# Kernel tuning notes

Measured on AMD Instinct MI355X. Metric: run time of the kernel, lower is better.

The kernel has to match this reference:

```python
import jax, jax.numpy as jnp
import numpy as np

D_MODEL = 1024
K = 256
AMPLITUDE_MAX = 3.0
GATE_BIAS_INIT = 0.65  # alpha-gate bias initialized at logit(0.65)


def setup_inputs() -> dict:
    key = jax.random.key(0)
    k0, k1, k2, k3 = jax.random.split(key, 4)
    B, n = 4, 4096
    x = jax.random.normal(k0, (B, n, D_MODEL), dtype=jnp.float32)
    # OscillatorProjection: Linear(d_model -> 6K), chunks [A, omega, phi, alpha, g, beta]
    W_proj = jax.random.normal(k1, (6 * K, D_MODEL), dtype=jnp.float32) * 0.02
    b_proj = jnp.zeros((6 * K,), dtype=jnp.float32)
    alpha_bias = float(np.log(GATE_BIAS_INIT / (1.0 - GATE_BIAS_INIT)))
    b_proj = b_proj.at[3 * K:4 * K].set(alpha_bias)
    W_res = jax.random.normal(k2, (D_MODEL, 4 * K - 2), dtype=jnp.float32) * 0.002
    W_phase = jax.random.normal(k3, (K, D_MODEL), dtype=jnp.float32) * 0.001
    b_phase = jnp.zeros((K,), dtype=jnp.float32)
    return {
        "x": x, "W_proj": W_proj, "b_proj": b_proj, "W_res": W_res,
        "W_phase": W_phase, "b_phase": b_phase,
        "lambda_pcg": jnp.float32(0.1), "res_scale": jnp.float32(0.05),
    }


def _scan_combine(c1, c2):
    # first-order linear recurrence r_t = a_t * r_{t-1} + b_t (complex, split re/im)
    a1, br1, bi1 = c1
    a2, br2, bi2 = c2
    return (a1 * a2, a2 * br1 + br2, a2 * bi1 + bi2)


def _forward(x, W_proj, b_proj, W_res, W_phase, b_phase, lambda_pcg, res_scale):
    B, n, _ = x.shape
    # OscillatorProjection
    proj = jnp.einsum('bnd,kd->bnk', x, W_proj) + b_proj  # (B, n, 6K)
    a_raw, w_raw, p_raw, al_raw, g_raw, be_raw = jnp.split(proj, 6, axis=-1)
    A = AMPLITUDE_MAX * jax.nn.sigmoid(a_raw)
    omega = jax.nn.softplus(w_raw)
    phi = p_raw
    alpha = jax.nn.sigmoid(al_raw)
    g_out = jax.nn.sigmoid(g_raw)
    beta = jax.nn.sigmoid(be_raw)

    # phase_mode == 'log'
    positions = jnp.log1p(jnp.arange(n, dtype=jnp.float32)).reshape(1, n, 1)
    angle = omega * positions + phi
    cos_a = jnp.cos(angle)
    sin_a = jnp.sin(angle)
    one_m_a = 1.0 - alpha
    drive_r = one_m_a * A * cos_a
    drive_i = one_m_a * A * sin_a

    # parallel associative prefix scan over sequence axis
    _, r_r, r_i = jax.lax.associative_scan(_scan_combine, (alpha, drive_r, drive_i), axis=1)

    # erase (read-and-subtract)
    readout = r_r * cos_a + r_i * sin_a
    r_r = r_r - beta * readout * cos_a
    r_i = r_i - beta * readout * sin_a

    # state norm: r /= max(|r|, 1)
    modulus = jnp.sqrt(r_r * r_r + r_i * r_i + 1e-8)
    scale = jnp.maximum(modulus, 1.0)
    r_r = r_r / scale
    r_i = r_i / scale

    # demodulate: rho = r * exp(-j * angle)
    rho_re = r_r * cos_a + r_i * sin_a
    rho_im = -r_r * sin_a + r_i * cos_a

    # phase-coherence gate
    rho_norm = jnp.sqrt(rho_re * rho_re + rho_im * rho_im + 1e-8)
    phase_query = jnp.einsum('bnd,kd->bnk', x, W_phase) + b_phase
    phase_alignment = (rho_re / rho_norm) * jnp.cos(phase_query) + (rho_im / rho_norm) * jnp.sin(phase_query)
    phase_gate = jax.nn.sigmoid(lambda_pcg * phase_alignment)
    rho_re = phase_gate * rho_re
    rho_im = phase_gate * rho_im

    # SCPM: neighbor complex cross-products
    xcross_re = rho_re[:, :, :-1] * rho_re[:, :, 1:] - rho_im[:, :, :-1] * rho_im[:, :, 1:]
    xcross_im = rho_re[:, :, :-1] * rho_im[:, :, 1:] + rho_im[:, :, :-1] * rho_re[:, :, 1:]
    rho_base = jnp.concatenate([rho_re, rho_im], axis=-1)              # (B, n, 2K)
    g_base = jnp.concatenate([g_out, g_out], axis=-1)
    g_cross = 0.5 * (g_out[:, :, :-1] + g_out[:, :, 1:])
    xcross = jnp.concatenate([xcross_re, xcross_im], axis=-1)          # (B, n, 2K-2)
    g_cross_full = jnp.concatenate([g_cross, g_cross], axis=-1)
    rho = jnp.concatenate([g_base * rho_base, g_cross_full * xcross], axis=-1)  # (B, n, 4K-2)

    # eval mode: warmup_factor == 1.0
    return res_scale * jnp.einsum('bnk,dk->bnd', rho, W_res)


def reference(x, W_proj, b_proj, W_res, W_phase, b_phase, lambda_pcg, res_scale):
    return _forward(x, W_proj, b_proj, W_res, W_phase, b_phase, lambda_pcg, res_scale)
```

## Files before the change

### kernel.cpp

```cpp
#include <hip/hip_runtime.h>
#include <cmath>

#define D_MODEL 1024
#define KOSC    256
#define NSEQ    4096
#define BATCH   4
#define NROW    (BATCH * NSEQ)
#define JTOT    1792

typedef short      s16x8 __attribute__((ext_vector_type(8)));
typedef float      f32x4 __attribute__((ext_vector_type(4)));

#define GL2LDS(gsrc, ldst)                                                      \
  __builtin_amdgcn_global_load_lds(                                             \
      (const __attribute__((address_space(1))) unsigned int*)(gsrc),            \
      (__attribute__((address_space(3))) unsigned int*)(ldst), 16, 0, 0)

__device__ __forceinline__ float sigm(float x) {
    return 1.0f / (1.0f + expf(-x));
}
__device__ __forceinline__ float softplusf_(float x) {
    return fmaxf(x, 0.0f) + log1pf(expf(-fabsf(x)));
}

__device__ __forceinline__ void bf16_split(float f, unsigned short& hi,
                                           unsigned short& lo) {
    unsigned u = __float_as_uint(f);
    unsigned r = u + 0x7FFFu + ((u >> 16) & 1u);
    hi = (unsigned short)(r >> 16);
    float fh = __uint_as_float((unsigned)hi << 16);
    float fl = f - fh;
    unsigned ul = __float_as_uint(fl);
    unsigned rl = ul + 0x7FFFu + ((ul >> 16) & 1u);
    lo = (unsigned short)(rl >> 16);
}

__global__ __launch_bounds__(256) void split_x_kernel(
    const float* __restrict__ x, unsigned short* __restrict__ XH,
    unsigned short* __restrict__ XL)
{
    int i = blockIdx.x * 256 + threadIdx.x;
    float4 v = ((const float4*)x)[i];
    ushort4 h, l;
    bf16_split(v.x, h.x, l.x);
    bf16_split(v.y, h.y, l.y);
    bf16_split(v.z, h.z, l.z);
    bf16_split(v.w, h.w, l.w);
    ((ushort4*)XH)[i] = h;
    ((ushort4*)XL)[i] = l;
}

__global__ __launch_bounds__(256) void split_w_kernel(
    const float* __restrict__ Wproj, const float* __restrict__ Wphase,
    unsigned short* __restrict__ WH, unsigned short* __restrict__ WL)
{
    int i = blockIdx.x * 256 + threadIdx.x;
    int elem = i << 2;
    int row = elem >> 10;
    int col = elem & 1023;
    const float* src = (row < 1536) ? (Wproj + (size_t)row * 1024 + col)
                                    : (Wphase + (size_t)(row - 1536) * 1024 + col);
    float4 v = *(const float4*)src;
    ushort4 h, l;
    bf16_split(v.x, h.x, l.x);
    bf16_split(v.y, h.y, l.y);
    bf16_split(v.z, h.z, l.z);
    bf16_split(v.w, h.w, l.w);
    ((ushort4*)WH)[i] = h;
    ((ushort4*)WL)[i] = l;
}

__global__ __launch_bounds__(256) void pack_wres_kernel(
    const float* __restrict__ Wres, unsigned short* __restrict__ WPH)
{
    int idx = blockIdx.x * 256 + threadIdx.x;
    int d = idx >> 10;
    int j = idx & 1023;
    float v = (j < 1022) ? Wres[(size_t)d * 1022 + j] : 0.0f;
    unsigned u = __float_as_uint(v);
    unsigned r = u + 0x7FFFu + ((u >> 16) & 1u);
    WPH[idx] = (unsigned short)(r >> 16);
}

__global__ __launch_bounds__(256, 3) void gemm1_full_kernel(
    const unsigned short* __restrict__ WH, const unsigned short* __restrict__ WL,
    const unsigned short* __restrict__ XH, const unsigned short* __restrict__ XL,
    const float* __restrict__ bproj, float* __restrict__ PT)
{
    __shared__ __attribute__((aligned(16))) unsigned short AH[4096];
    __shared__ __attribute__((aligned(16))) unsigned short AL[4096];
    __shared__ __attribute__((aligned(16))) unsigned short BH[4096];
    __shared__ __attribute__((aligned(16))) unsigned short BL[4096];

    const int tid  = threadIdx.x;
    const int lane = tid & 63;
    const int w    = tid >> 6;
    const int wm   = w >> 1, wn = w & 1;
    const int m0   = (blockIdx.y + 2) * 128;
    const int n0   = blockIdx.x * 128;
    const int fr   = lane & 15;
    const int fq   = lane >> 4;

    f32x4 acc[4][4];
    #pragma unroll
    for (int i = 0; i < 4; i++)
        #pragma unroll
        for (int j = 0; j < 4; j++) acc[i][j] = (f32x4){0.f, 0.f, 0.f, 0.f};

    for (int kc = 0; kc < 32; kc++) {
        const int kbase = kc * 32;
        __syncthreads();
        #pragma unroll
        for (int t = 0; t < 2; t++) {
            int G  = w * 128 + t * 64 + lane;
            int gm = G & 127;
            int gq = G >> 7;
            size_t offA = (size_t)(m0 + gm) * 1024 + kbase + gq * 8;
            size_t offB = (size_t)(n0 + gm) * 1024 + kbase + gq * 8;
            int ldsg = (w * 128 + t * 64) * 8;
            GL2LDS(WH + offA, &AH[ldsg]);
            GL2LDS(WL + offA, &AL[ldsg]);
            GL2LDS(XH + offB, &BH[ldsg]);
            GL2LDS(XL + offB, &BL[ldsg]);
        }
        __syncthreads();

        s16x8 ah[4], al[4], bh[4], bl[4];
        #pragma unroll
        for (int f = 0; f < 4; f++) {
            int aoff = (fq * 128 + wm * 64 + f * 16 + fr) * 8;
            int boff = (fq * 128 + wn * 64 + f * 16 + fr) * 8;
            ah[f] = *(const s16x8*)&AH[aoff];
            al[f] = *(const s16x8*)&AL[aoff];
            bh[f] = *(const s16x8*)&BH[boff];
            bl[f] = *(const s16x8*)&BL[boff];
        }
        #pragma unroll
        for (int i = 0; i < 4; i++)
            #pragma unroll
            for (int j = 0; j < 4; j++) {
                acc[i][j] = __builtin_amdgcn_mfma_f32_16x16x32_bf16(ah[i], bh[j], acc[i][j], 0, 0, 0);
                acc[i][j] = __builtin_amdgcn_mfma_f32_16x16x32_bf16(ah[i], bl[j], acc[i][j], 0, 0, 0);
                acc[i][j] = __builtin_amdgcn_mfma_f32_16x16x32_bf16(al[i], bh[j], acc[i][j], 0, 0, 0);
            }
    }

    #pragma unroll
    for (int i = 0; i < 4; i++) {
        int mbase = m0 + wm * 64 + i * 16 + fq * 4;
        #pragma unroll
        for (int j = 0; j < 4; j++) {
            int n = n0 + wn * 64 + j * 16 + fr;
            #pragma unroll
            for (int rg = 0; rg < 4; rg++) {
                int m = mbase + rg;
                PT[(size_t)m * NROW + n] = acc[i][j][rg] + bproj[m];
            }
        }
    }
}

__global__ __launch_bounds__(256, 4) void gemm1_lite_kernel(
    const unsigned short* __restrict__ WH, const unsigned short* __restrict__ XH,
    const float* __restrict__ bproj, const float* __restrict__ bphase,
    float* __restrict__ PT)
{
    __shared__ __attribute__((aligned(16))) unsigned short AH[8192];
    __shared__ __attribute__((aligned(16))) unsigned short BH[8192];

    const int tid  = threadIdx.x;
    const int lane = tid & 63;
    const int w    = tid >> 6;
    const int wm   = w >> 1, wn = w & 1;
    const int yt   = blockIdx.y;
    const int jt   = (yt < 2) ? yt : yt + 4;
    const int m0   = jt * 128;
    const int n0   = blockIdx.x * 128;
    const int fr   = lane & 15;
    const int fq   = lane >> 4;

    f32x4 acc[4][4];
    #pragma unroll
    for (int i = 0; i < 4; i++)
        #pragma unroll
        for (int j = 0; j < 4; j++) acc[i][j] = (f32x4){0.f, 0.f, 0.f, 0.f};

    for (int kc = 0; kc < 16; kc++) {
        const int kbase = kc * 64;
        __syncthreads();
        #pragma unroll
        for (int t = 0; t < 4; t++) {
            int G  = t * 256 + tid;
            int gm = G & 127;
            int gq = G >> 7;
            size_t offA = (size_t)(m0 + gm) * 1024 + kbase + gq * 8;
            size_t offB = (size_t)(n0 + gm) * 1024 + kbase + gq * 8;
            int ldsg = (t * 256 + w * 64) * 8;
            GL2LDS(WH + offA, &AH[ldsg]);
            GL2LDS(XH + offB, &BH[ldsg]);
        }
        __syncthreads();

        #pragma unroll
        for (int s = 0; s < 2; s++) {
            s16x8 ah[4], bh[4];
            #pragma unroll
            for (int f = 0; f < 4; f++) {
                int aoff = (((s * 4 + fq) * 128) + wm * 64 + f * 16 + fr) * 8;
                int boff = (((s * 4 + fq) * 128) + wn * 64 + f * 16 + fr) * 8;
                ah[f] = *(const s16x8*)&AH[aoff];
                bh[f] = *(const s16x8*)&BH[boff];
            }
            #pragma unroll
            for (int i = 0; i < 4; i++)
                #pragma unroll
                for (int j = 0; j < 4; j++)
                    acc[i][j] = __builtin_amdgcn_mfma_f32_16x16x32_bf16(ah[i], bh[j], acc[i][j], 0, 0, 0);
        }
    }

    #pragma unroll
    for (int i = 0; i < 4; i++) {
        int mbase = m0 + wm * 64 + i * 16 + fq * 4;
        #pragma unroll
        for (int j = 0; j < 4; j++) {
            int n = n0 + wn * 64 + j * 16 + fr;
            #pragma unroll
            for (int rg = 0; rg < 4; rg++) {
                int m = mbase + rg;
                float bias = (m < 1536) ? bproj[m] : bphase[m - 1536];
                PT[(size_t)m * NROW + n] = acc[i][j][rg] + bias;
            }
        }
    }
}

__global__ __launch_bounds__(256) void scan_kernel(float* PT,
                                                   const float* lambda_ptr)
{
    const int bx = blockIdx.x;
    const int k = bx & 255;
    const int b = bx >> 8;
    const int t = threadIdx.x;
    const size_t colb = (size_t)b * NSEQ;
    const size_t R = NROW;

    float* rowA  = PT + (size_t)(k)        * R + colb;
    float* rowW  = PT + (size_t)(256 + k)  * R + colb;
    float* rowP  = PT + (size_t)(512 + k)  * R + colb;
    float* rowAl = PT + (size_t)(768 + k)  * R + colb;
    float* rowG  = PT + (size_t)(1024 + k) * R + colb;
    float* rowBe = PT + (size_t)(1280 + k) * R + colb;
    float* rowPq = PT + (size_t)(1536 + k) * R + colb;

    __shared__ float s_al[NSEQ + 256];
    __shared__ float s_rr[NSEQ + 256];
    __shared__ float s_ri[NSEQ + 256];
    __shared__ float s_sa[256], s_sbr[256], s_sbi[256];

    const float lam = *lambda_ptr;

    float cs_r[16], sn_r[16];

    #pragma unroll
    for (int i = 0; i < 16; i++) {
        int n = i * 256 + t;
        float araw = rowA[n];
        float wraw = rowW[n];
        float praw = rowP[n];
        float alraw = rowAl[n];
        float A     = 3.0f * sigm(araw);
        float alpha = sigm(alraw);
        float omega = softplusf_(wraw);
        float ang   = fmaf(omega, log1pf((float)n), praw);
        float sn, cs;
        sincosf(ang, &sn, &cs);
        cs_r[i] = cs;
        sn_r[i] = sn;
        float amp = (1.0f - alpha) * A;
        int pidx = n + (n >> 4);
        s_al[pidx] = alpha;
        s_rr[pidx] = amp * cs;
        s_ri[pidx] = amp * sn;
    }
    __syncthreads();

    {
        float ap = 1.0f, br = 0.0f, bi = 0.0f;
        int base = t * 17;
        #pragma unroll
        for (int i = 0; i < 16; i++) {
            float a = s_al[base + i];
            br = fmaf(a, br, s_rr[base + i]);
            bi = fmaf(a, bi, s_ri[base + i]);
            ap *= a;
        }
        s_sa[t] = ap; s_sbr[t] = br; s_sbi[t] = bi;
    }
    __syncthreads();

    for (int off = 1; off < 256; off <<= 1) {
        float a2 = s_sa[t], b2r = s_sbr[t], b2i = s_sbi[t];
        float a1 = 1.0f, b1r = 0.0f, b1i = 0.0f;
        if (t >= off) { a1 = s_sa[t - off]; b1r = s_sbr[t - off]; b1i = s_sbi[t - off]; }
        __syncthreads();
        s_sa[t]  = a1 * a2;
        s_sbr[t] = fmaf(a2, b1r, b2r);
        s_sbi[t] = fmaf(a2, b1i, b2i);
        __syncthreads();
    }

    {
        float cr = 0.0f, ci = 0.0f;
        if (t > 0) { cr = s_sbr[t - 1]; ci = s_sbi[t - 1]; }
        int base = t * 17;
        #pragma unroll
        for (int i = 0; i < 16; i++) {
            float a = s_al[base + i];
            cr = fmaf(a, cr, s_rr[base + i]);
            ci = fmaf(a, ci, s_ri[base + i]);
            s_rr[base + i] = cr;
            s_ri[base + i] = ci;
        }
    }
    __syncthreads();

    #pragma unroll
    for (int i = 0; i < 16; i++) {
        int n = i * 256 + t;
        float beraw = rowBe[n];
        float graw = rowG[n];
        float pq = rowPq[n];

        float cs = cs_r[i];
        float sn = sn_r[i];

        int pidx = n + (n >> 4);
        float rr = s_rr[pidx], ri = s_ri[pidx];
        float beta = sigm(beraw);
        float g = sigm(graw);

        float readout = rr * cs + ri * sn;
        rr -= beta * readout * cs;
        ri -= beta * readout * sn;

        float modulus = sqrtf(rr * rr + ri * ri + 1e-8f);
        float scale = fmaxf(modulus, 1.0f);
        rr /= scale; ri /= scale;

        float rho_re = rr * cs + ri * sn;
        float rho_im = -rr * sn + ri * cs;

        float rho_norm = sqrtf(rho_re * rho_re + rho_im * rho_im + 1e-8f);
        float sq, cq;
        sincosf(pq, &sq, &cq);
        float pa = (rho_re * cq + rho_im * sq) / rho_norm;
        float gate = sigm(lam * pa);
        rho_re *= gate;
        rho_im *= gate;

        rowA[n] = rho_re;
        rowW[n] = rho_im;
        rowP[n] = g;
    }
}

__global__ __launch_bounds__(256) void pack_rho_kernel(
    const float* __restrict__ PT, unsigned short* __restrict__ RTH,
    unsigned short* __restrict__ RTL)
{
    __shared__ float s_re[256 * 33];
    __shared__ float s_im[256 * 33];
    __shared__ float s_g [256 * 33];

    const int tid = threadIdx.x;
    const int r0 = blockIdx.x * 32;

    {
        int lr = tid & 31;
        int k0 = tid >> 5;
        for (int it = 0; it < 32; it++) {
            int k = it * 8 + k0;
            size_t go = (size_t)k * NROW + r0 + lr;
            s_re[k * 33 + lr] = PT[go];
            s_im[k * 33 + lr] = PT[(size_t)256 * NROW + go];
            s_g [k * 33 + lr] = PT[(size_t)512 * NROW + go];
        }
    }
    __syncthreads();

    const int r = tid >> 3;
    const int c = tid & 7;
    for (int i = 0; i < 16; i++) {
        int jb = (c + 8 * i) * 8;
        unsigned short h[8], l[8];
        #pragma unroll
        for (int e = 0; e < 8; e++) {
            int j = jb + e;
            float v;
            if (j < 256) {
                v = s_g[j * 33 + r] * s_re[j * 33 + r];
            } else if (j < 512) {
                int k = j - 256;
                v = s_g[k * 33 + r] * s_im[k * 33 + r];
            } else if (j < 767) {
                int k = j - 512;
                float gc = 0.5f * (s_g[k * 33 + r] + s_g[(k + 1) * 33 + r]);
                v = gc * (s_re[k * 33 + r] * s_re[(k + 1) * 33 + r]
                        - s_im[k * 33 + r] * s_im[(k + 1) * 33 + r]);
            } else if (j < 1022) {
                int k = j - 767;
                float gc = 0.5f * (s_g[k * 33 + r] + s_g[(k + 1) * 33 + r]);
                v = gc * (s_re[k * 33 + r] * s_im[(k + 1) * 33 + r]
                        + s_im[k * 33 + r] * s_re[(k + 1) * 33 + r]);
            } else {
                v = 0.0f;
            }
            bf16_split(v, h[e], l[e]);
        }
        size_t off = (size_t)(r0 + r) * 1024 + jb;
        s16x8 hv, lv;
        #pragma unroll
        for (int e = 0; e < 8; e++) { hv[e] = (short)h[e]; lv[e] = (short)l[e]; }
        *(s16x8*)&RTH[off] = hv;
        *(s16x8*)&RTL[off] = lv;
    }
}

__global__ __launch_bounds__(256, 3) void gemm2_kernel(
    const unsigned short* __restrict__ WPH,
    const unsigned short* __restrict__ RTH, const unsigned short* __restrict__ RTL,
    const float* __restrict__ rs_ptr, float* __restrict__ out)
{
    __shared__ __attribute__((aligned(16))) unsigned short AH[4096];
    __shared__ __attribute__((aligned(16))) unsigned short BH[4096];
    __shared__ __attribute__((aligned(16))) unsigned short BL[4096];

    const int tid  = threadIdx.x;
    const int lane = tid & 63;
    const int w    = tid >> 6;
    const int wm   = w >> 1, wn = w & 1;
    const int m0   = blockIdx.y * 128;
    const int n0   = blockIdx.x * 128;
    const int fr   = lane & 15;
    const int fq   = lane >> 4;
    const float rs = *rs_ptr;

    f32x4 acc[4][4];
    #pragma unroll
    for (int i = 0; i < 4; i++)
        #pragma unroll
        for (int j = 0; j < 4; j++) acc[i][j] = (f32x4){0.f, 0.f, 0.f, 0.f};

    for (int kc = 0; kc < 32; kc++) {
        const int kbase = kc * 32;
        __syncthreads();
        #pragma unroll
        for (int t = 0; t < 2; t++) {
            int G  = w * 128 + t * 64 + lane;
            int gm = G & 127;
            int gq = G >> 7;
            size_t offA = (size_t)(m0 + gm) * 1024 + kbase + gq * 8;
            size_t offB = (size_t)(n0 + gm) * 1024 + kbase + gq * 8;
            int ldsg = (w * 128 + t * 64) * 8;
            GL2LDS(WPH + offA, &AH[ldsg]);
            GL2LDS(RTH + offB, &BH[ldsg]);
            GL2LDS(RTL + offB, &BL[ldsg]);
        }
        __syncthreads();

        s16x8 ah[4], bh[4], bl[4];
        #pragma unroll
        for (int f = 0; f < 4; f++) {
            int aoff = (fq * 128 + wm * 64 + f * 16 + fr) * 8;
            int boff = (fq * 128 + wn * 64 + f * 16 + fr) * 8;
            ah[f] = *(const s16x8*)&AH[aoff];
            bh[f] = *(const s16x8*)&BH[boff];
            bl[f] = *(const s16x8*)&BL[boff];
        }
        #pragma unroll
        for (int i = 0; i < 4; i++)
            #pragma unroll
            for (int j = 0; j < 4; j++) {
                acc[i][j] = __builtin_amdgcn_mfma_f32_16x16x32_bf16(ah[i], bh[j], acc[i][j], 0, 0, 0);
                acc[i][j] = __builtin_amdgcn_mfma_f32_16x16x32_bf16(ah[i], bl[j], acc[i][j], 0, 0, 0);
            }
    }

    #pragma unroll
    for (int i = 0; i < 4; i++) {
        int d = m0 + wm * 64 + i * 16 + fq * 4;
        #pragma unroll
        for (int j = 0; j < 4; j++) {
            int n = n0 + wn * 64 + j * 16 + fr;
            float4 v = { rs * acc[i][j][0], rs * acc[i][j][1],
                         rs * acc[i][j][2], rs * acc[i][j][3] };
            *(float4*)&out[(size_t)n * 1024 + d] = v;
        }
    }
}

extern "C" void kernel_launch(void* const* d_in, const int* in_sizes, int n_in,
                              void* d_out, int out_size, void* d_ws, size_t ws_size,
                              hipStream_t stream)
{
    const float* x      = (const float*)d_in[0];
    const float* Wproj  = (const float*)d_in[1];
    const float* bproj  = (const float*)d_in[2];
    const float* Wres   = (const float*)d_in[3];
    const float* Wphase = (const float*)d_in[4];
    const float* bphase = (const float*)d_in[5];
    const float* lam    = (const float*)d_in[6];
    const float* rs     = (const float*)d_in[7];
    float* out = (float*)d_out;

    float* PT = (float*)d_ws;
    unsigned short* WH  = (unsigned short*)((char*)d_ws + (size_t)JTOT * NROW * 4);
    unsigned short* WL  = WH + (size_t)JTOT * 1024;
    unsigned short* RTH = (unsigned short*)(PT + (size_t)768 * NROW);
    unsigned short* RTL = RTH + (size_t)NROW * 1024;
    unsigned short* WPH = (unsigned short*)PT;
    unsigned short* XH  = (unsigned short*)d_out;
    unsigned short* XL  = XH + (size_t)NROW * 1024;

    hipLaunchKernelGGL(split_x_kernel, dim3(NROW * D_MODEL / 1024), dim3(256), 0, stream,
                       x, XH, XL);
    hipLaunchKernelGGL(split_w_kernel, dim3(JTOT * D_MODEL / 1024), dim3(256), 0, stream,
                       Wproj, Wphase, WH, WL);
    hipLaunchKernelGGL(gemm1_full_kernel, dim3(NROW / 128, 4), dim3(256), 0, stream,
                       WH, WL, XH, XL, bproj, PT);
    hipLaunchKernelGGL(gemm1_lite_kernel, dim3(NROW / 128, 10), dim3(256), 0, stream,
                       WH, XH, bproj, bphase, PT);
    hipLaunchKernelGGL(scan_kernel, dim3(BATCH * KOSC), dim3(256), 0, stream,
                       PT, lam);
    hipLaunchKernelGGL(pack_rho_kernel, dim3(NROW / 32), dim3(256), 0, stream,
                       PT, RTH, RTL);
    hipLaunchKernelGGL(pack_wres_kernel, dim3(1024 * 1024 / 256), dim3(256), 0, stream,
                       Wres, WPH);
    hipLaunchKernelGGL(gemm2_kernel, dim3(NROW / 128, 1024 / 128), dim3(256), 0, stream,
                       WPH, RTH, RTL, rs, out);
}
```

Before: 532.8 us.

## Double-buffer LDS tiles in all three GEMM kernels with MFMA priority boost

Switches the three MFMA GEMM kernels from single-buffered LDS staging, which had two barriers per k-step, to double buffering. The next k-tile is issued via global_load_lds while the current tile is consumed, leaving one barrier per step. s_setprio raises wave priority around the MFMA blocks. LDS use per block doubles and launch bounds drop to 2 blocks per CU, which lowers occupancy. Correctness relies on the async LDS loads completing before the end-of-iteration barrier.

```diff
diff --git a/kernel.cpp b/kernel.cpp
--- a/kernel.cpp
+++ b/kernel.cpp
@@ -82,15 +82,15 @@
     WPH[idx] = (unsigned short)(r >> 16);
 }
 
-__global__ __launch_bounds__(256, 3) void gemm1_full_kernel(
+__global__ __launch_bounds__(256, 2) void gemm1_full_kernel(
     const unsigned short* __restrict__ WH, const unsigned short* __restrict__ WL,
     const unsigned short* __restrict__ XH, const unsigned short* __restrict__ XL,
     const float* __restrict__ bproj, float* __restrict__ PT)
 {
-    __shared__ __attribute__((aligned(16))) unsigned short AH[4096];
-    __shared__ __attribute__((aligned(16))) unsigned short AL[4096];
-    __shared__ __attribute__((aligned(16))) unsigned short BH[4096];
-    __shared__ __attribute__((aligned(16))) unsigned short BL[4096];
+    __shared__ __attribute__((aligned(16))) unsigned short AH[8192];
+    __shared__ __attribute__((aligned(16))) unsigned short AL[8192];
+    __shared__ __attribute__((aligned(16))) unsigned short BH[8192];
+    __shared__ __attribute__((aligned(16))) unsigned short BL[8192];
 
     const int tid  = threadIdx.x;
     const int lane = tid & 63;
@@ -107,9 +107,8 @@
         #pragma unroll
         for (int j = 0; j < 4; j++) acc[i][j] = (f32x4){0.f, 0.f, 0.f, 0.f};
 
-    for (int kc = 0; kc < 32; kc++) {
+    auto STAGE = [&](int buf, int kc) {
         const int kbase = kc * 32;
-        __syncthreads();
         #pragma unroll
         for (int t = 0; t < 2; t++) {
             int G  = w * 128 + t * 64 + lane;
@@ -117,24 +116,32 @@
             int gq = G >> 7;
             size_t offA = (size_t)(m0 + gm) * 1024 + kbase + gq * 8;
             size_t offB = (size_t)(n0 + gm) * 1024 + kbase + gq * 8;
-            int ldsg = (w * 128 + t * 64) * 8;
+            int ldsg = buf * 4096 + (w * 128 + t * 64) * 8;
             GL2LDS(WH + offA, &AH[ldsg]);
             GL2LDS(WL + offA, &AL[ldsg]);
             GL2LDS(XH + offB, &BH[ldsg]);
             GL2LDS(XL + offB, &BL[ldsg]);
         }
-        __syncthreads();
+    };
+
+    STAGE(0, 0);
+    __syncthreads();
+
+    for (int kc = 0; kc < 32; kc++) {
+        const int cur = kc & 1;
+        if (kc + 1 < 32) STAGE(cur ^ 1, kc + 1);
 
         s16x8 ah[4], al[4], bh[4], bl[4];
         #pragma unroll
         for (int f = 0; f < 4; f++) {
-            int aoff = (fq * 128 + wm * 64 + f * 16 + fr) * 8;
-            int boff = (fq * 128 + wn * 64 + f * 16 + fr) * 8;
+            int aoff = cur * 4096 + (fq * 128 + wm * 64 + f * 16 + fr) * 8;
+            int boff = cur * 4096 + (fq * 128 + wn * 64 + f * 16 + fr) * 8;
             ah[f] = *(const s16x8*)&AH[aoff];
             al[f] = *(const s16x8*)&AL[aoff];
             bh[f] = *(const s16x8*)&BH[boff];
             bl[f] = *(const s16x8*)&BL[boff];
         }
+        __builtin_amdgcn_s_setprio(1);
         #pragma unroll
         for (int i = 0; i < 4; i++)
             #pragma unroll
@@ -143,6 +150,8 @@
                 acc[i][j] = __builtin_amdgcn_mfma_f32_16x16x32_bf16(ah[i], bl[j], acc[i][j], 0, 0, 0);
                 acc[i][j] = __builtin_amdgcn_mfma_f32_16x16x32_bf16(al[i], bh[j], acc[i][j], 0, 0, 0);
             }
+        __builtin_amdgcn_s_setprio(0);
+        __syncthreads();
     }
 
     #pragma unroll
@@ -160,13 +169,13 @@
     }
 }
 
-__global__ __launch_bounds__(256, 4) void gemm1_lite_kernel(
+__global__ __launch_bounds__(256, 2) void gemm1_lite_kernel(
     const unsigned short* __restrict__ WH, const unsigned short* __restrict__ XH,
     const float* __restrict__ bproj, const float* __restrict__ bphase,
     float* __restrict__ PT)
 {
-    __shared__ __attribute__((aligned(16))) unsigned short AH[8192];
-    __shared__ __attribute__((aligned(16))) unsigned short BH[8192];
+    __shared__ __attribute__((aligned(16))) unsigned short AH[16384];
+    __shared__ __attribute__((aligned(16))) unsigned short BH[16384];
 
     const int tid  = threadIdx.x;
     const int lane = tid & 63;
@@ -185,9 +194,8 @@
         #pragma unroll
         for (int j = 0; j < 4; j++) acc[i][j] = (f32x4){0.f, 0.f, 0.f, 0.f};
 
-    for (int kc = 0; kc < 16; kc++) {
+    auto STAGE = [&](int buf, int kc) {
         const int kbase = kc * 64;
-        __syncthreads();
         #pragma unroll
         for (int t = 0; t < 4; t++) {
             int G  = t * 256 + tid;
@@ -195,28 +203,38 @@
             int gq = G >> 7;
             size_t offA = (size_t)(m0 + gm) * 1024 + kbase + gq * 8;
             size_t offB = (size_t)(n0 + gm) * 1024 + kbase + gq * 8;
-            int ldsg = (t * 256 + w * 64) * 8;
+            int ldsg = buf * 8192 + (t * 256 + w * 64) * 8;
             GL2LDS(WH + offA, &AH[ldsg]);
             GL2LDS(XH + offB, &BH[ldsg]);
         }
-        __syncthreads();
+    };
+
+    STAGE(0, 0);
+    __syncthreads();
+
+    for (int kc = 0; kc < 16; kc++) {
+        const int cur = kc & 1;
+        if (kc + 1 < 16) STAGE(cur ^ 1, kc + 1);
 
         #pragma unroll
         for (int s = 0; s < 2; s++) {
             s16x8 ah[4], bh[4];
             #pragma unroll
             for (int f = 0; f < 4; f++) {
-                int aoff = (((s * 4 + fq) * 128) + wm * 64 + f * 16 + fr) * 8;
-                int boff = (((s * 4 + fq) * 128) + wn * 64 + f * 16 + fr) * 8;
+                int aoff = cur * 8192 + (((s * 4 + fq) * 128) + wm * 64 + f * 16 + fr) * 8;
+                int boff = cur * 8192 + (((s * 4 + fq) * 128) + wn * 64 + f * 16 + fr) * 8;
                 ah[f] = *(const s16x8*)&AH[aoff];
                 bh[f] = *(const s16x8*)&BH[boff];
             }
+            __builtin_amdgcn_s_setprio(1);
             #pragma unroll
             for (int i = 0; i < 4; i++)
                 #pragma unroll
                 for (int j = 0; j < 4; j++)
                     acc[i][j] = __builtin_amdgcn_mfma_f32_16x16x32_bf16(ah[i], bh[j], acc[i][j], 0, 0, 0);
-        }
+            __builtin_amdgcn_s_setprio(0);
+        }
+        __syncthreads();
     }
 
     #pragma unroll
@@ -432,9 +450,9 @@
     const unsigned short* __restrict__ RTH, const unsigned short* __restrict__ RTL,
     const float* __restrict__ rs_ptr, float* __restrict__ out)
 {
-    __shared__ __attribute__((aligned(16))) unsigned short AH[4096];
-    __shared__ __attribute__((aligned(16))) unsigned short BH[4096];
-    __shared__ __attribute__((aligned(16))) unsigned short BL[4096];
+    __shared__ __attribute__((aligned(16))) unsigned short AH[8192];
+    __shared__ __attribute__((aligned(16))) unsigned short BH[8192];
+    __shared__ __attribute__((aligned(16))) unsigned short BL[8192];
 
     const int tid  = threadIdx.x;
     const int lane = tid & 63;
@@ -452,9 +470,8 @@
         #pragma unroll
         for (int j = 0; j < 4; j++) acc[i][j] = (f32x4){0.f, 0.f, 0.f, 0.f};
 
-    for (int kc = 0; kc < 32; kc++) {
+    auto STAGE = [&](int buf, int kc) {
         const int kbase = kc * 32;
-        __syncthreads();
         #pragma unroll
         for (int t = 0; t < 2; t++) {
             int G  = w * 128 + t * 64 + lane;
@@ -462,22 +479,30 @@
             int gq = G >> 7;
             size_t offA = (size_t)(m0 + gm) * 1024 + kbase + gq * 8;
             size_t offB = (size_t)(n0 + gm) * 1024 + kbase + gq * 8;
-            int ldsg = (w * 128 + t * 64) * 8;
+            int ldsg = buf * 4096 + (w * 128 + t * 64) * 8;
             GL2LDS(WPH + offA, &AH[ldsg]);
             GL2LDS(RTH + offB, &BH[ldsg]);
             GL2LDS(RTL + offB, &BL[ldsg]);
         }
-        __syncthreads();
+    };
+
+    STAGE(0, 0);
+    __syncthreads();
+
+    for (int kc = 0; kc < 32; kc++) {
+        const int cur = kc & 1;
+        if (kc + 1 < 32) STAGE(cur ^ 1, kc + 1);
 
         s16x8 ah[4], bh[4], bl[4];
         #pragma unroll
         for (int f = 0; f < 4; f++) {
-            int aoff = (fq * 128 + wm * 64 + f * 16 + fr) * 8;
-            int boff = (fq * 128 + wn * 64 + f * 16 + fr) * 8;
+            int aoff = cur * 4096 + (fq * 128 + wm * 64 + f * 16 + fr) * 8;
+            int boff = cur * 4096 + (fq * 128 + wn * 64 + f * 16 + fr) * 8;
             ah[f] = *(const s16x8*)&AH[aoff];
             bh[f] = *(const s16x8*)&BH[boff];
             bl[f] = *(const s16x8*)&BL[boff];
         }
+        __builtin_amdgcn_s_setprio(1);
         #pragma unroll
         for (int i = 0; i < 4; i++)
             #pragma unroll
@@ -485,6 +510,8 @@
                 acc[i][j] = __builtin_amdgcn_mfma_f32_16x16x32_bf16(ah[i], bh[j], acc[i][j], 0, 0, 0);
                 acc[i][j] = __builtin_amdgcn_mfma_f32_16x16x32_bf16(ah[i], bl[j], acc[i][j], 0, 0, 0);
             }
+        __builtin_amdgcn_s_setprio(0);
+        __syncthreads();
     }
 
     #pragma unroll
```

New measurement: 534.2 us. About the same (+0.3%).

## Rewrite scan kernel with register-resident chunks and wavefront shuffle prefix scan

Applied to the files above, without the earlier changes.

Each thread now owns 16 contiguous sequence elements, loaded and stored as float4 vectors, and keeps them in registers instead of staging through LDS. The block-level Hillis-Steele scan with many __syncthreads is replaced by a 64-lane shuffle scan plus a small cross-wave combine through four shared slots. This removes most LDS traffic and barriers. It raises register pressure, which the launch bound of 3 blocks per unit tries to cap, at the risk of spills. Per-thread global accesses become strided by 16 elements rather than coalesced across threads.

```diff
diff --git a/kernel.cpp b/kernel.cpp
--- a/kernel.cpp
+++ b/kernel.cpp
@@ -235,110 +235,110 @@
     }
 }
 
-__global__ __launch_bounds__(256) void scan_kernel(float* PT,
-                                                   const float* lambda_ptr)
+__global__ __launch_bounds__(256, 3) void scan_kernel(float* PT,
+                                                      const float* lambda_ptr)
 {
     const int bx = blockIdx.x;
     const int k = bx & 255;
     const int b = bx >> 8;
     const int t = threadIdx.x;
+    const int lane = t & 63;
+    const int wv = t >> 6;
     const size_t colb = (size_t)b * NSEQ;
     const size_t R = NROW;
-
-    float* rowA  = PT + (size_t)(k)        * R + colb;
-    float* rowW  = PT + (size_t)(256 + k)  * R + colb;
-    float* rowP  = PT + (size_t)(512 + k)  * R + colb;
-    float* rowAl = PT + (size_t)(768 + k)  * R + colb;
-    float* rowG  = PT + (size_t)(1024 + k) * R + colb;
-    float* rowBe = PT + (size_t)(1280 + k) * R + colb;
-    float* rowPq = PT + (size_t)(1536 + k) * R + colb;
-
-    __shared__ float s_al[NSEQ + 256];
-    __shared__ float s_rr[NSEQ + 256];
-    __shared__ float s_ri[NSEQ + 256];
-    __shared__ float s_sa[256], s_sbr[256], s_sbi[256];
+    const int n0 = t * 16;
+
+    float* rowA  = PT + (size_t)(k)        * R + colb + n0;
+    float* rowW  = PT + (size_t)(256 + k)  * R + colb + n0;
+    float* rowP  = PT + (size_t)(512 + k)  * R + colb + n0;
+    float* rowAl = PT + (size_t)(768 + k)  * R + colb + n0;
+    float* rowG  = PT + (size_t)(1024 + k) * R + colb + n0;
+    float* rowBe = PT + (size_t)(1280 + k) * R + colb + n0;
+    float* rowPq = PT + (size_t)(1536 + k) * R + colb + n0;
+
+    __shared__ float s_a[4], s_br[4], s_bi[4];
 
     const float lam = *lambda_ptr;
 
-    float cs_r[16], sn_r[16];
-
+    float al_r[16], rr_r[16], ri_r[16], cs_r[16], sn_r[16];
+
+    float fa[16], fw[16], fp[16], fl[16];
+    #pragma unroll
+    for (int q = 0; q < 4; q++) {
+        *(float4*)&fa[q * 4] = ((const float4*)rowA)[q];
+        *(float4*)&fw[q * 4] = ((const float4*)rowW)[q];
+        *(float4*)&fp[q * 4] = ((const float4*)rowP)[q];
+        *(float4*)&fl[q * 4] = ((const float4*)rowAl)[q];
+    }
+    float ap = 1.0f, br = 0.0f, bi = 0.0f;
     #pragma unroll
     for (int i = 0; i < 16; i++) {
-        int n = i * 256 + t;
-        float araw = rowA[n];
-        float wraw = rowW[n];
-        float praw = rowP[n];
-        float alraw = rowAl[n];
-        float A     = 3.0f * sigm(araw);
-        float alpha = sigm(alraw);
-        float omega = softplusf_(wraw);
-        float ang   = fmaf(omega, log1pf((float)n), praw);
+        float A     = 3.0f * sigm(fa[i]);
+        float alpha = sigm(fl[i]);
+        float omega = softplusf_(fw[i]);
+        float ang   = fmaf(omega, log1pf((float)(n0 + i)), fp[i]);
         float sn, cs;
         sincosf(ang, &sn, &cs);
-        cs_r[i] = cs;
-        sn_r[i] = sn;
         float amp = (1.0f - alpha) * A;
-        int pidx = n + (n >> 4);
-        s_al[pidx] = alpha;
-        s_rr[pidx] = amp * cs;
-        s_ri[pidx] = amp * sn;
-    }
+        float dr = amp * cs, di = amp * sn;
+        al_r[i] = alpha; cs_r[i] = cs; sn_r[i] = sn;
+        rr_r[i] = dr;    ri_r[i] = di;
+        br = fmaf(alpha, br, dr);
+        bi = fmaf(alpha, bi, di);
+        ap *= alpha;
+    }
+
+    #pragma unroll
+    for (int off = 1; off < 64; off <<= 1) {
+        float pa  = __shfl_up(ap, off);
+        float pbr = __shfl_up(br, off);
+        float pbi = __shfl_up(bi, off);
+        if (lane >= off) {
+            br = fmaf(ap, pbr, br);
+            bi = fmaf(ap, pbi, bi);
+            ap *= pa;
+        }
+    }
+
+    if (lane == 63) { s_a[wv] = ap; s_br[wv] = br; s_bi[wv] = bi; }
     __syncthreads();
-
-    {
-        float ap = 1.0f, br = 0.0f, bi = 0.0f;
-        int base = t * 17;
-        #pragma unroll
-        for (int i = 0; i < 16; i++) {
-            float a = s_al[base + i];
-            br = fmaf(a, br, s_rr[base + i]);
-            bi = fmaf(a, bi, s_ri[base + i]);
-            ap *= a;
-        }
-        s_sa[t] = ap; s_sbr[t] = br; s_sbi[t] = bi;
-    }
-    __syncthreads();
-
-    for (int off = 1; off < 256; off <<= 1) {
-        float a2 = s_sa[t], b2r = s_sbr[t], b2i = s_sbi[t];
-        float a1 = 1.0f, b1r = 0.0f, b1i = 0.0f;
-        if (t >= off) { a1 = s_sa[t - off]; b1r = s_sbr[t - off]; b1i = s_sbi[t - off]; }
-        __syncthreads();
-        s_sa[t]  = a1 * a2;
-        s_sbr[t] = fmaf(a2, b1r, b2r);
-        s_sbi[t] = fmaf(a2, b1i, b2i);
-        __syncthreads();
-    }
-
-    {
-        float cr = 0.0f, ci = 0.0f;
-        if (t > 0) { cr = s_sbr[t - 1]; ci = s_sbi[t - 1]; }
-        int base = t * 17;
-        #pragma unroll
-        for (int i = 0; i < 16; i++) {
-            float a = s_al[base + i];
-            cr = fmaf(a, cr, s_rr[base + i]);
-            ci = fmaf(a, ci, s_ri[base + i]);
-            s_rr[base + i] = cr;
-            s_ri[base + i] = ci;
-        }
-    }
-    __syncthreads();
+    float cbr = 0.0f, cbi = 0.0f;
+    #pragma unroll
+    for (int u = 0; u < 3; u++) {
+        if (u < wv) {
+            cbr = fmaf(s_a[u], cbr, s_br[u]);
+            cbi = fmaf(s_a[u], cbi, s_bi[u]);
+        }
+    }
+    float ea  = __shfl_up(ap, 1);
+    float ebr = __shfl_up(br, 1);
+    float ebi = __shfl_up(bi, 1);
+    if (lane == 0) { ea = 1.0f; ebr = 0.0f; ebi = 0.0f; }
+    float cr = fmaf(ea, cbr, ebr);
+    float ci = fmaf(ea, cbi, ebi);
 
     #pragma unroll
     for (int i = 0; i < 16; i++) {
-        int n = i * 256 + t;
-        float beraw = rowBe[n];
-        float graw = rowG[n];
-        float pq = rowPq[n];
-
-        float cs = cs_r[i];
-        float sn = sn_r[i];
-
-        int pidx = n + (n >> 4);
-        float rr = s_rr[pidx], ri = s_ri[pidx];
-        float beta = sigm(beraw);
-        float g = sigm(graw);
+        cr = fmaf(al_r[i], cr, rr_r[i]);
+        ci = fmaf(al_r[i], ci, ri_r[i]);
+        rr_r[i] = cr;
+        ri_r[i] = ci;
+    }
+
+    float fbe[16], fg[16], fq_[16];
+    #pragma unroll
+    for (int q = 0; q < 4; q++) {
+        *(float4*)&fbe[q * 4] = ((const float4*)rowBe)[q];
+        *(float4*)&fg[q * 4]  = ((const float4*)rowG)[q];
+        *(float4*)&fq_[q * 4] = ((const float4*)rowPq)[q];
+    }
+    float ore[16], oim[16], og[16];
+    #pragma unroll
+    for (int i = 0; i < 16; i++) {
+        float cs = cs_r[i], sn = sn_r[i];
+        float rr = rr_r[i], ri = ri_r[i];
+        float beta = sigm(fbe[i]);
+        float g = sigm(fg[i]);
 
         float readout = rr * cs + ri * sn;
         rr -= beta * readout * cs;
@@ -353,15 +353,18 @@
 
         float rho_norm = sqrtf(rho_re * rho_re + rho_im * rho_im + 1e-8f);
         float sq, cq;
-        sincosf(pq, &sq, &cq);
-        float pa = (rho_re * cq + rho_im * sq) / rho_norm;
-        float gate = sigm(lam * pa);
-        rho_re *= gate;
-        rho_im *= gate;
-
-        rowA[n] = rho_re;
-        rowW[n] = rho_im;
-        rowP[n] = g;
+        sincosf(fq_[i], &sq, &cq);
+        float pa2 = (rho_re * cq + rho_im * sq) / rho_norm;
+        float gate = sigm(lam * pa2);
+        ore[i] = gate * rho_re;
+        oim[i] = gate * rho_im;
+        og[i]  = g;
+    }
+    #pragma unroll
+    for (int q = 0; q < 4; q++) {
+        ((float4*)rowA)[q] = *(const float4*)&ore[q * 4];
+        ((float4*)rowW)[q] = *(const float4*)&oim[q * 4];
+        ((float4*)rowP)[q] = *(const float4*)&og[q * 4];
     }
 }
 
```

Result: slower. 560.1 us (+5.1%).
